# Kernel tuning notes

Measured on AMD Instinct MI355X. Metric: run time of the kernel, lower is better.

Reference implementation:

```python
import jax, jax.numpy as jnp
import numpy as np

N = 50000          # nodes
E = 1_600_000      # edges (avg degree 32)
FEAT = 128         # nfeat == nhid
HID = 128
L = 3              # nconvs
C = 10             # nclass
G = 128            # graphs in batch
BN_EPS = 1e-5


def setup_inputs() -> dict:
    key = jax.random.key(0)
    ks = jax.random.split(key, 8)
    x = jax.random.normal(ks[0], (N, FEAT), dtype=jnp.float32)
    edge_index = jax.random.randint(ks[1], (2, E), 0, N, dtype=jnp.int64)
    batch = jnp.sort(jax.random.randint(ks[2], (N,), 0, G, dtype=jnp.int64))
    # stacked per-layer MLP params (nfeat == nhid so shapes are uniform)
    W1 = jax.random.normal(ks[3], (L, FEAT, HID), dtype=jnp.float32) * 0.05
    b1 = jnp.zeros((L, HID), dtype=jnp.float32)
    W2 = jax.random.normal(ks[4], (L, HID, HID), dtype=jnp.float32) * 0.05
    b2 = jnp.zeros((L, HID), dtype=jnp.float32)
    # BatchNorm (eval mode: running stats)
    gamma = jnp.ones((L, HID), dtype=jnp.float32)
    beta = jnp.zeros((L, HID), dtype=jnp.float32)
    rmean = jnp.zeros((L, HID), dtype=jnp.float32)
    rvar = jnp.ones((L, HID), dtype=jnp.float32)
    fc_w = jax.random.normal(ks[5], (HID, C), dtype=jnp.float32) * 0.05
    fc_b = jnp.zeros((C,), dtype=jnp.float32)
    return {
        "x": x, "edge_index": edge_index, "batch": batch,
        "W1": W1, "b1": b1, "W2": W2, "b2": b2,
        "gamma": gamma, "beta": beta, "rmean": rmean, "rvar": rvar,
        "fc_w": fc_w, "fc_b": fc_b,
    }


def reference(x, edge_index, batch, W1, b1, W2, b2, gamma, beta, rmean, rvar, fc_w, fc_b):
    src, dst = edge_index[0], edge_index[1]
    for l in range(L):
        # GINConv aggregation: h_i = (1 + eps) * x_i + sum_{j -> i} x_j  (eps = 0)
        agg = jax.ops.segment_sum(x[src], dst, num_segments=N)  # [N, d] scatter-add
        h = x + agg
        # MLP: Linear -> ReLU -> Linear -> BatchNorm (eval: running stats)
        h = jax.nn.relu(h @ W1[l] + b1[l])
        h = h @ W2[l] + b2[l]
        h = (h - rmean[l]) * jax.lax.rsqrt(rvar[l] + BN_EPS) * gamma[l] + beta[l]
        # outer ReLU; dropout is identity at inference
        x = jax.nn.relu(h)
    # global mean pool over batch ids
    counts = jax.ops.segment_sum(jnp.ones((N,), x.dtype), batch, num_segments=G)
    pooled = jax.ops.segment_sum(x, batch, num_segments=G)
    pooled = pooled / jnp.clip(counts, 1.0)[:, None]  # [G, HID]
    logits = pooled @ fc_w + fc_b                      # [G, C]
    return jax.nn.log_softmax(logits, axis=1)
```

## Files before the change

kernel.cpp:

```cpp
#include <hip/hip_runtime.h>

#define NN 50000
#define EE 1600000
#define GG 128
#define NC 10

#define SB_N   49
#define SB_PAD 36864
#define BK_N   782
#define BK_PAD 2560
#define CHUNK  4096
#define NBLK1  391
#define SLICES 9

typedef __attribute__((ext_vector_type(8))) short bf16x8;
typedef __attribute__((ext_vector_type(4))) float f32x4;
typedef unsigned short u16;

__device__ inline u16 f2bf(float x){
  unsigned u = __builtin_bit_cast(unsigned, x);
  u += 0x7fffu + ((u >> 16) & 1u);
  return (u16)(u >> 16);
}
__device__ inline float bf2f(u16 u){
  return __builtin_bit_cast(float, ((unsigned)u) << 16);
}

__global__ void k_zero_int(int* __restrict__ p, int n){
  int i = blockIdx.x * 256 + threadIdx.x;
  if (i < n) p[i] = 0;
}

__global__ __launch_bounds__(256) void k_scatL1(const int* __restrict__ srcI, const int* __restrict__ dstI,
                                                int* __restrict__ scur, int* __restrict__ sstg){
  __shared__ int hist[SB_N];
  __shared__ int base[64];
  __shared__ int gadj[SB_N];
  __shared__ unsigned reo[CHUNK];
  int t = threadIdx.x;
  int e0 = blockIdx.x * CHUNK;
  int cnt = EE - e0; if (cnt > CHUNK) cnt = CHUNK;
  if (t < SB_N) hist[t] = 0;
  __syncthreads();
  unsigned p[16]; int rk[16];
  #pragma unroll
  for (int r = 0; r < 16; ++r){
    int i = r * 256 + t;
    if (i < cnt){
      unsigned d = (unsigned)dstI[e0 + i];
      p[r] = (d << 16) | (unsigned)srcI[e0 + i];
      rk[r] = atomicAdd(&hist[d >> 10], 1);
    }
  }
  __syncthreads();
  if (t < 64) base[t] = (t < SB_N) ? hist[t] : 0;
  __syncthreads();
  for (int off = 1; off < 64; off <<= 1){
    int a = (t < 64 && t >= off) ? base[t - off] : 0;
    __syncthreads();
    if (t < 64) base[t] += a;
    __syncthreads();
  }
  if (t < SB_N){
    int ex = base[t] - hist[t];
    gadj[t] = atomicAdd(&scur[t], hist[t]) - ex;
  }
  __syncthreads();
  #pragma unroll
  for (int r = 0; r < 16; ++r){
    int i = r * 256 + t;
    if (i < cnt){
      unsigned sb = p[r] >> 26;
      reo[(base[sb] - hist[sb]) + rk[r]] = p[r];
    }
  }
  __syncthreads();
  for (int q = t; q < cnt; q += 256){
    unsigned v = reo[q];
    unsigned sb = v >> 26;
    int off = gadj[sb] + q;
    if ((unsigned)off < SB_PAD) sstg[sb * SB_PAD + off] = (int)v;
  }
}

__global__ __launch_bounds__(256) void k_scatL2(const int* __restrict__ sstg, const int* __restrict__ scur,
                                                int* __restrict__ bcur, int* __restrict__ bstg){
  __shared__ int hist[16];
  __shared__ int base[16];
  __shared__ int gadj[16];
  __shared__ unsigned reo[CHUNK];
  int t = threadIdx.x;
  int sb = blockIdx.x / SLICES;
  int sl = blockIdx.x % SLICES;
  int ssz = scur[sb]; if (ssz > SB_PAD) ssz = SB_PAD;
  int i0 = sl * CHUNK;
  int cnt = ssz - i0;
  if (cnt <= 0) return;
  if (cnt > CHUNK) cnt = CHUNK;
  if (t < 16) hist[t] = 0;
  __syncthreads();
  unsigned p[16]; int rk[16];
  #pragma unroll
  for (int r = 0; r < 16; ++r){
    int i = r * 256 + t;
    if (i < cnt){
      p[r] = (unsigned)sstg[sb * SB_PAD + i0 + i];
      rk[r] = atomicAdd(&hist[(p[r] >> 22) & 15], 1);
    }
  }
  __syncthreads();
  if (t < 16) base[t] = hist[t];
  __syncthreads();
  for (int off = 1; off < 16; off <<= 1){
    int a = (t < 16 && t >= off) ? base[t - off] : 0;
    __syncthreads();
    if (t < 16) base[t] += a;
    __syncthreads();
  }
  if (t < 16){
    int ex = base[t] - hist[t];
    gadj[t] = atomicAdd(&bcur[sb * 16 + t], hist[t]) - ex;
  }
  __syncthreads();
  #pragma unroll
  for (int r = 0; r < 16; ++r){
    int i = r * 256 + t;
    if (i < cnt){
      unsigned b = (p[r] >> 22) & 15;
      reo[(base[b] - hist[b]) + rk[r]] = p[r];
    }
  }
  __syncthreads();
  for (int q = t; q < cnt; q += 256){
    unsigned v = reo[q];
    unsigned b = (v >> 22) & 15;
    int off = gadj[b] + q;
    if ((unsigned)off < BK_PAD) bstg[(sb * 16 + b) * BK_PAD + off] = (int)v;
  }
}

__global__ __launch_bounds__(256) void k_finalize(const int* __restrict__ bstg, const int* __restrict__ bcur,
                                                  u16* __restrict__ adj, int2* __restrict__ ndinfo){
  __shared__ unsigned ebuf[BK_PAD];
  __shared__ int hist[64];
  __shared__ int lrs[64];
  __shared__ int lcur[64];
  int b = blockIdx.x;
  int t = threadIdx.x;
  int bsz = bcur[b]; if (bsz > BK_PAD) bsz = BK_PAD;
  if (t < 64) hist[t] = 0;
  __syncthreads();
  for (int i = t; i < bsz; i += 256){
    unsigned p = (unsigned)bstg[b * BK_PAD + i];
    ebuf[i] = p;
    atomicAdd(&hist[(p >> 16) & 63], 1);
  }
  __syncthreads();
  if (t < 64) lrs[t] = hist[t];
  __syncthreads();
  for (int off = 1; off < 64; off <<= 1){
    int a = (t < 64 && t >= off) ? lrs[t - off] : 0;
    __syncthreads();
    if (t < 64) lrs[t] += a;
    __syncthreads();
  }
  if (t < 64){
    int ex = lrs[t] - hist[t];
    lcur[t] = ex;
    int node = b * 64 + t;
    if (node < NN) ndinfo[node] = make_int2(b * BK_PAD + ex, hist[t]);
  }
  __syncthreads();
  for (int i = t; i < bsz; i += 256){
    unsigned p = ebuf[i];
    int slot = atomicAdd(&lcur[(p >> 16) & 63], 1);
    adj[b * BK_PAD + slot] = (u16)(p & 0xffffu);
  }
}

__global__ void k_cvt_x(const float* __restrict__ x, u16* __restrict__ xb){
  int i = blockIdx.x * 256 + threadIdx.x;
  float4 v = ((const float4*)x)[i];
  ushort4 o;
  o.x = f2bf(v.x); o.y = f2bf(v.y); o.z = f2bf(v.z); o.w = f2bf(v.w);
  ((ushort4*)xb)[i] = o;
}

__global__ void k_prep_w(const float* __restrict__ W1, const float* __restrict__ W2,
                         u16* __restrict__ Wt){
  int i = blockIdx.x * 256 + threadIdx.x;
  int a = i >> 14; int r = i & 16383; int n = r >> 7; int k = r & 127;
  const float* Wsrc = (a < 3) ? (W1 + a * 16384) : (W2 + (a - 3) * 16384);
  Wt[a * 16384 + n * 128 + k] = f2bf(Wsrc[k * 128 + n]);
}

__global__ void k_prep_scsh(const float* __restrict__ b1, const float* __restrict__ b2,
                            const float* __restrict__ gma, const float* __restrict__ bta,
                            const float* __restrict__ rmn, const float* __restrict__ rvr,
                            float* __restrict__ SC, float* __restrict__ SH){
  int i = blockIdx.x * 256 + threadIdx.x;
  if (i < 768){
    int l = i >> 8; int r = i & 255; int mode = r >> 7; int c = r & 127;
    if (mode == 0){
      SC[(l * 2) * 128 + c] = 1.0f;
      SH[(l * 2) * 128 + c] = b1[l * 128 + c];
    } else {
      float S = gma[l * 128 + c] * rsqrtf(rvr[l * 128 + c] + 1e-5f);
      SC[(l * 2 + 1) * 128 + c] = S;
      SH[(l * 2 + 1) * 128 + c] = (b2[l * 128 + c] - rmn[l * 128 + c]) * S + bta[l * 128 + c];
    }
  }
}

__global__ __launch_bounds__(256) void k_agg(const u16* __restrict__ xb, u16* __restrict__ hb,
                                             const u16* __restrict__ adj,
                                             const int2* __restrict__ ndinfo){
  int t = threadIdx.x;
  int node = blockIdx.x * 16 + (t >> 4);
  int lane = t & 15;
  const bf16x8* xv = (const bf16x8*)xb;
  bf16x8 sv = xv[(long)node * 16 + lane];
  float a[8];
  #pragma unroll
  for (int j = 0; j < 8; ++j) a[j] = bf2f((u16)sv[j]);
  int2 nd = ndinfo[node];
  int r0 = nd.x;
  int d  = nd.y;
  int j = 0;
  for (; j + 4 <= d; j += 4){
    int s0 = adj[r0 + j + 0];
    int s1 = adj[r0 + j + 1];
    int s2 = adj[r0 + j + 2];
    int s3 = adj[r0 + j + 3];
    bf16x8 v0 = xv[(long)s0 * 16 + lane];
    bf16x8 v1 = xv[(long)s1 * 16 + lane];
    bf16x8 v2 = xv[(long)s2 * 16 + lane];
    bf16x8 v3 = xv[(long)s3 * 16 + lane];
    #pragma unroll
    for (int q = 0; q < 8; ++q)
      a[q] += bf2f((u16)v0[q]) + bf2f((u16)v1[q]) + bf2f((u16)v2[q]) + bf2f((u16)v3[q]);
  }
  for (; j < d; ++j){
    int s0 = adj[r0 + j];
    bf16x8 v0 = xv[(long)s0 * 16 + lane];
    #pragma unroll
    for (int q = 0; q < 8; ++q) a[q] += bf2f((u16)v0[q]);
  }
  bf16x8 o;
  #pragma unroll
  for (int j2 = 0; j2 < 8; ++j2) o[j2] = (short)f2bf(a[j2]);
  ((bf16x8*)hb)[(long)node * 16 + lane] = o;
}

__global__ __launch_bounds__(256, 2) void k_gemm(const u16* __restrict__ Ain,
                                                 const u16* __restrict__ Wt,
                                                 const float* __restrict__ SC,
                                                 const float* __restrict__ SH,
                                                 u16* __restrict__ Out){
  int gw = (blockIdx.x * 256 + threadIdx.x) >> 6;
  int l  = threadIdx.x & 63;
  int m  = l & 15;
  int kb = l >> 4;
  const int NW = (gridDim.x * 256) >> 6;

  bf16x8 w[8][4];
  #pragma unroll
  for (int mt = 0; mt < 8; ++mt)
    #pragma unroll
    for (int ks = 0; ks < 4; ++ks)
      w[mt][ks] = *(const bf16x8*)(Wt + (mt * 16 + m) * 128 + ks * 32 + kb * 8);

  for (int tile = gw; tile < 3125; tile += NW){
    long row0 = (long)tile * 16;
    f32x4 acc[8] = {};
    #pragma unroll
    for (int ks = 0; ks < 4; ++ks){
      bf16x8 h = *(const bf16x8*)(Ain + (row0 + m) * 128 + ks * 32 + kb * 8);
      #pragma unroll
      for (int mt = 0; mt < 8; ++mt)
        acc[mt] = __builtin_amdgcn_mfma_f32_16x16x32_bf16(w[mt][ks], h, acc[mt], 0, 0, 0);
    }
    #pragma unroll
    for (int mt = 0; mt < 8; ++mt){
      int c0 = mt * 16 + kb * 4;
      float4 sc = *(const float4*)(SC + c0);
      float4 sh = *(const float4*)(SH + c0);
      float v0 = fmaxf(acc[mt][0] * sc.x + sh.x, 0.f);
      float v1 = fmaxf(acc[mt][1] * sc.y + sh.y, 0.f);
      float v2 = fmaxf(acc[mt][2] * sc.z + sh.z, 0.f);
      float v3 = fmaxf(acc[mt][3] * sc.w + sh.w, 0.f);
      ushort4 o;
      o.x = f2bf(v0); o.y = f2bf(v1); o.z = f2bf(v2); o.w = f2bf(v3);
      *(ushort4*)(Out + (row0 + m) * 128 + c0) = o;
    }
  }
}

__global__ __launch_bounds__(256) void k_pool(const u16* __restrict__ xb,
                                              const int* __restrict__ batch,
                                              float* __restrict__ pooled){
  __shared__ float4 red[8][32];
  int b = blockIdx.x;
  int n0 = b << 6;
  int t = threadIdx.x;
  int lane = t & 31;
  int rg = t >> 5;
  int g0 = batch[n0];
  int lastn = n0 + 63; if (lastn >= NN) lastn = NN - 1;
  int nk = batch[lastn] - g0;
  const ushort4* xv = (const ushort4*)xb;
  float4 a0 = {0,0,0,0}, a1 = {0,0,0,0}, a2 = {0,0,0,0};
  int rbase = n0 + rg * 8;
  #pragma unroll
  for (int i = 0; i < 8; ++i){
    int r = rbase + i;
    if (r >= NN) break;
    int k = batch[r] - g0;
    ushort4 v = xv[(long)r * 32 + lane];
    float fx = bf2f(v.x), fy = bf2f(v.y), fz = bf2f(v.z), fw = bf2f(v.w);
    if (k == 0){ a0.x += fx; a0.y += fy; a0.z += fz; a0.w += fw; }
    else if (k == 1){ a1.x += fx; a1.y += fy; a1.z += fz; a1.w += fw; }
    else if (k == 2){ a2.x += fx; a2.y += fy; a2.z += fz; a2.w += fw; }
    else {
      float* pg = pooled + (g0 + k) * 128 + lane * 4;
      atomicAdd(pg + 0, fx); atomicAdd(pg + 1, fy);
      atomicAdd(pg + 2, fz); atomicAdd(pg + 3, fw);
    }
  }
  int kmax = (nk < 2) ? nk : 2;
  for (int k = 0; k <= kmax; ++k){
    red[rg][lane] = (k == 0) ? a0 : ((k == 1) ? a1 : a2);
    __syncthreads();
    if (t < 32){
      float4 s = red[0][t];
      #pragma unroll
      for (int r = 1; r < 8; ++r){
        float4 q = red[r][t];
        s.x += q.x; s.y += q.y; s.z += q.z; s.w += q.w;
      }
      float* pg = pooled + (g0 + k) * 128 + t * 4;
      atomicAdd(pg + 0, s.x); atomicAdd(pg + 1, s.y);
      atomicAdd(pg + 2, s.z); atomicAdd(pg + 3, s.w);
    }
    __syncthreads();
  }
}

__global__ void k_head(const float* __restrict__ pooled, const float* __restrict__ fcw,
                       const float* __restrict__ fcb, const int* __restrict__ batch,
                       float* __restrict__ out){
  int g = threadIdx.x;
  int lo, hi;
  { int a = 0, b = NN; while (a < b){ int mm = (a + b) >> 1; if (batch[mm] < g) a = mm + 1; else b = mm; } lo = a; }
  { int a = lo, b = NN; while (a < b){ int mm = (a + b) >> 1; if (batch[mm] < g + 1) a = mm + 1; else b = mm; } hi = a; }
  float inv = 1.0f / fmaxf((float)(hi - lo), 1.0f);
  float logit[NC];
  #pragma unroll
  for (int c = 0; c < NC; ++c) logit[c] = fcb[c];
  for (int k = 0; k < 128; ++k){
    float pv = pooled[g * 128 + k] * inv;
    #pragma unroll
    for (int c = 0; c < NC; ++c) logit[c] += pv * fcw[k * NC + c];
  }
  float m = logit[0];
  #pragma unroll
  for (int c = 1; c < NC; ++c) m = fmaxf(m, logit[c]);
  float sum = 0.f;
  #pragma unroll
  for (int c = 0; c < NC; ++c) sum += expf(logit[c] - m);
  float ls = logf(sum);
  #pragma unroll
  for (int c = 0; c < NC; ++c) out[g * NC + c] = logit[c] - m - ls;
}

extern "C" void kernel_launch(void* const* d_in, const int* in_sizes, int n_in,
                              void* d_out, int out_size, void* d_ws, size_t ws_size,
                              hipStream_t stream) {
  const float* x     = (const float*)d_in[0];
  const int*   eidx  = (const int*)  d_in[1];
  const int*   batch = (const int*)  d_in[2];
  const float* W1    = (const float*)d_in[3];
  const float* b1    = (const float*)d_in[4];
  const float* W2    = (const float*)d_in[5];
  const float* b2    = (const float*)d_in[6];
  const float* gma   = (const float*)d_in[7];
  const float* bta   = (const float*)d_in[8];
  const float* rmn   = (const float*)d_in[9];
  const float* rvr   = (const float*)d_in[10];
  const float* fcw   = (const float*)d_in[11];
  const float* fcb   = (const float*)d_in[12];
  float* out = (float*)d_out;

  const int* srcI = eidx;
  const int* dstI = eidx + EE;

  u16* bufX = (u16*)d_ws;
  u16* bufA = bufX + 6400000;
  u16* bufB = bufA + 6400000;
  u16* Wt   = bufB + 6400000;
  float* SC = (float*)(Wt + 98304);
  float* SH = SC + 768;
  float* pooled = SH + 768;
  int* ctr  = (int*)(pooled + 16384);
  int* scur = ctr;
  int* bcur = ctr + 64;
  u16* adj  = (u16*)(ctr + 848);
  int2* ndinfo = (int2*)(adj + (BK_N * BK_PAD));
  int* sstg = (int*)bufA;
  int* bstg = (int*)bufB;

  k_zero_int<<<68, 256, 0, stream>>>((int*)pooled, 16384 + 848);

  k_scatL1  <<<NBLK1, 256, 0, stream>>>(srcI, dstI, scur, sstg);
  k_scatL2  <<<SB_N * SLICES, 256, 0, stream>>>(sstg, scur, bcur, bstg);
  k_finalize<<<BK_N, 256, 0, stream>>>(bstg, bcur, adj, ndinfo);

  k_cvt_x    <<<6250, 256, 0, stream>>>(x, bufX);
  k_prep_w   <<<384, 256, 0, stream>>>(W1, W2, Wt);
  k_prep_scsh<<<3, 256, 0, stream>>>(b1, b2, gma, bta, rmn, rvr, SC, SH);

  u16* aggin [3] = { bufX, bufA, bufB };
  u16* aggout[3] = { bufA, bufB, bufA };
  u16* g0out [3] = { bufB, bufX, bufX };
  u16* g1out [3] = { bufA, bufB, bufA };

  for (int l = 0; l < 3; ++l){
    k_agg <<<3125, 256, 0, stream>>>(aggin[l], aggout[l], adj, ndinfo);
    k_gemm<<<256, 256, 0, stream>>>(aggout[l], Wt + l * 16384,
                                    SC + (l * 2) * 128, SH + (l * 2) * 128, g0out[l]);
    k_gemm<<<256, 256, 0, stream>>>(g0out[l], Wt + (3 + l) * 16384,
                                    SC + (l * 2 + 1) * 128, SH + (l * 2 + 1) * 128, g1out[l]);
  }

  k_pool<<<BK_N, 256, 0, stream>>>(g1out[2], batch, pooled);
  k_head<<<1, 128, 0, stream>>>(pooled, fcw, fcb, batch, out);
}
```

Baseline: 416.5 us.

## Fuse both MLP GEMMs per layer with pooling and merge prep kernels

Result: slower. 473.0 us (+13.6%).

```diff
diff --git a/kernel.cpp b/kernel.cpp
--- a/kernel.cpp
+++ b/kernel.cpp
@@ -178,36 +178,36 @@
   }
 }
 
-__global__ void k_cvt_x(const float* __restrict__ x, u16* __restrict__ xb){
-  int i = blockIdx.x * 256 + threadIdx.x;
-  float4 v = ((const float4*)x)[i];
-  ushort4 o;
-  o.x = f2bf(v.x); o.y = f2bf(v.y); o.z = f2bf(v.z); o.w = f2bf(v.w);
-  ((ushort4*)xb)[i] = o;
-}
-
-__global__ void k_prep_w(const float* __restrict__ W1, const float* __restrict__ W2,
-                         u16* __restrict__ Wt){
-  int i = blockIdx.x * 256 + threadIdx.x;
-  int a = i >> 14; int r = i & 16383; int n = r >> 7; int k = r & 127;
-  const float* Wsrc = (a < 3) ? (W1 + a * 16384) : (W2 + (a - 3) * 16384);
-  Wt[a * 16384 + n * 128 + k] = f2bf(Wsrc[k * 128 + n]);
-}
-
-__global__ void k_prep_scsh(const float* __restrict__ b1, const float* __restrict__ b2,
-                            const float* __restrict__ gma, const float* __restrict__ bta,
-                            const float* __restrict__ rmn, const float* __restrict__ rvr,
-                            float* __restrict__ SC, float* __restrict__ SH){
-  int i = blockIdx.x * 256 + threadIdx.x;
-  if (i < 768){
-    int l = i >> 8; int r = i & 255; int mode = r >> 7; int c = r & 127;
-    if (mode == 0){
-      SC[(l * 2) * 128 + c] = 1.0f;
-      SH[(l * 2) * 128 + c] = b1[l * 128 + c];
-    } else {
-      float S = gma[l * 128 + c] * rsqrtf(rvr[l * 128 + c] + 1e-5f);
-      SC[(l * 2 + 1) * 128 + c] = S;
-      SH[(l * 2 + 1) * 128 + c] = (b2[l * 128 + c] - rmn[l * 128 + c]) * S + bta[l * 128 + c];
+__global__ void k_prep(const float* __restrict__ x, const float* __restrict__ W1f, const float* __restrict__ W2f,
+                       const float* __restrict__ b1, const float* __restrict__ b2,
+                       const float* __restrict__ gma, const float* __restrict__ bta,
+                       const float* __restrict__ rmn, const float* __restrict__ rvr,
+                       u16* __restrict__ xb, u16* __restrict__ Wt,
+                       float* __restrict__ SC, float* __restrict__ SH){
+  int bid = blockIdx.x;
+  int t = threadIdx.x;
+  if (bid < 6250){
+    int i = bid * 256 + t;
+    float4 v = ((const float4*)x)[i];
+    ushort4 o;
+    o.x = f2bf(v.x); o.y = f2bf(v.y); o.z = f2bf(v.z); o.w = f2bf(v.w);
+    ((ushort4*)xb)[i] = o;
+  } else if (bid < 6634){
+    int i = (bid - 6250) * 256 + t;
+    int a = i >> 14; int r = i & 16383; int n = r >> 7; int k = r & 127;
+    const float* Wsrc = (a < 3) ? (W1f + a * 16384) : (W2f + (a - 3) * 16384);
+    Wt[a * 16384 + n * 128 + k] = f2bf(Wsrc[k * 128 + n]);
+  } else {
+    for (int i = t; i < 768; i += 256){
+      int l = i >> 8; int r = i & 255; int mode = r >> 7; int c = r & 127;
+      if (mode == 0){
+        SC[(l * 2) * 128 + c] = 1.0f;
+        SH[(l * 2) * 128 + c] = b1[l * 128 + c];
+      } else {
+        float S = gma[l * 128 + c] * rsqrtf(rvr[l * 128 + c] + 1e-5f);
+        SC[(l * 2 + 1) * 128 + c] = S;
+        SH[(l * 2 + 1) * 128 + c] = (b2[l * 128 + c] - rmn[l * 128 + c]) * S + bta[l * 128 + c];
+      }
     }
   }
 }
@@ -227,22 +227,33 @@
   int r0 = nd.x;
   int d  = nd.y;
   int j = 0;
+  for (; j + 8 <= d; j += 8){
+    bf16x8 v[8];
+    #pragma unroll
+    for (int u = 0; u < 8; ++u){
+      int s = adj[r0 + j + u];
+      v[u] = xv[(long)s * 16 + lane];
+    }
+    #pragma unroll
+    for (int q = 0; q < 8; ++q){
+      float s01 = bf2f((u16)v[0][q]) + bf2f((u16)v[1][q]);
+      float s23 = bf2f((u16)v[2][q]) + bf2f((u16)v[3][q]);
+      float s45 = bf2f((u16)v[4][q]) + bf2f((u16)v[5][q]);
+      float s67 = bf2f((u16)v[6][q]) + bf2f((u16)v[7][q]);
+      a[q] += (s01 + s23) + (s45 + s67);
+    }
+  }
   for (; j + 4 <= d; j += 4){
-    int s0 = adj[r0 + j + 0];
-    int s1 = adj[r0 + j + 1];
-    int s2 = adj[r0 + j + 2];
-    int s3 = adj[r0 + j + 3];
-    bf16x8 v0 = xv[(long)s0 * 16 + lane];
-    bf16x8 v1 = xv[(long)s1 * 16 + lane];
-    bf16x8 v2 = xv[(long)s2 * 16 + lane];
-    bf16x8 v3 = xv[(long)s3 * 16 + lane];
+    bf16x8 v0 = xv[(long)adj[r0 + j + 0] * 16 + lane];
+    bf16x8 v1 = xv[(long)adj[r0 + j + 1] * 16 + lane];
+    bf16x8 v2 = xv[(long)adj[r0 + j + 2] * 16 + lane];
+    bf16x8 v3 = xv[(long)adj[r0 + j + 3] * 16 + lane];
     #pragma unroll
     for (int q = 0; q < 8; ++q)
-      a[q] += bf2f((u16)v0[q]) + bf2f((u16)v1[q]) + bf2f((u16)v2[q]) + bf2f((u16)v3[q]);
+      a[q] += (bf2f((u16)v0[q]) + bf2f((u16)v1[q])) + (bf2f((u16)v2[q]) + bf2f((u16)v3[q]));
   }
   for (; j < d; ++j){
-    int s0 = adj[r0 + j];
-    bf16x8 v0 = xv[(long)s0 * 16 + lane];
+    bf16x8 v0 = xv[(long)adj[r0 + j] * 16 + lane];
     #pragma unroll
     for (int q = 0; q < 8; ++q) a[q] += bf2f((u16)v0[q]);
   }
@@ -252,23 +263,48 @@
   ((bf16x8*)hb)[(long)node * 16 + lane] = o;
 }
 
-__global__ __launch_bounds__(256, 2) void k_gemm(const u16* __restrict__ Ain,
-                                                 const u16* __restrict__ Wt,
-                                                 const float* __restrict__ SC,
-                                                 const float* __restrict__ SH,
-                                                 u16* __restrict__ Out){
-  int gw = (blockIdx.x * 256 + threadIdx.x) >> 6;
-  int l  = threadIdx.x & 63;
+template<int POOL>
+__global__ __launch_bounds__(256, 2) void k_mlp(const u16* __restrict__ Ain,
+                                                const u16* __restrict__ Wt1,
+                                                const u16* __restrict__ Wt2,
+                                                const float* __restrict__ B1,
+                                                const float* __restrict__ SC2,
+                                                const float* __restrict__ SH2,
+                                                const int* __restrict__ batch,
+                                                u16* __restrict__ Out,
+                                                float* __restrict__ pooled){
+  __shared__ u16 W2s[16384];
+  __shared__ u16 Hs[4][16][128];
+  __shared__ float P1[128], P2[128], P3[128];
+  int t = threadIdx.x;
+
+  #pragma unroll
+  for (int i = 0; i < 8; ++i){
+    int c = t + 256 * i;
+    int r = c >> 4, cc = c & 15;
+    unsigned byte = (unsigned)(r * 256 + cc * 16) ^ (unsigned)((r & 7) << 4);
+    *(bf16x8*)((char*)W2s + byte) = *(const bf16x8*)(Wt2 + c * 8);
+  }
+  if (t < 128){ P1[t] = B1[t]; P2[t] = SC2[t]; P3[t] = SH2[t]; }
+
+  int wv = t >> 6;
+  int l  = t & 63;
   int m  = l & 15;
   int kb = l >> 4;
-  const int NW = (gridDim.x * 256) >> 6;
-
-  bf16x8 w[8][4];
+
+  bf16x8 w1[8][4];
   #pragma unroll
   for (int mt = 0; mt < 8; ++mt)
     #pragma unroll
     for (int ks = 0; ks < 4; ++ks)
-      w[mt][ks] = *(const bf16x8*)(Wt + (mt * 16 + m) * 128 + ks * 32 + kb * 8);
+      w1[mt][ks] = *(const bf16x8*)(Wt1 + (mt * 16 + m) * 128 + ks * 32 + kb * 8);
+
+  __syncthreads();
+
+  char* hs = (char*)&Hs[wv][0][0];
+  unsigned mswz = (unsigned)((m & 7) << 4);
+  int gw = blockIdx.x * 4 + wv;
+  const int NW = gridDim.x * 4;
 
   for (int tile = gw; tile < 3125; tile += NW){
     long row0 = (long)tile * 16;
@@ -278,71 +314,86 @@
       bf16x8 h = *(const bf16x8*)(Ain + (row0 + m) * 128 + ks * 32 + kb * 8);
       #pragma unroll
       for (int mt = 0; mt < 8; ++mt)
-        acc[mt] = __builtin_amdgcn_mfma_f32_16x16x32_bf16(w[mt][ks], h, acc[mt], 0, 0, 0);
+        acc[mt] = __builtin_amdgcn_mfma_f32_16x16x32_bf16(w1[mt][ks], h, acc[mt], 0, 0, 0);
     }
     #pragma unroll
     for (int mt = 0; mt < 8; ++mt){
       int c0 = mt * 16 + kb * 4;
-      float4 sc = *(const float4*)(SC + c0);
-      float4 sh = *(const float4*)(SH + c0);
-      float v0 = fmaxf(acc[mt][0] * sc.x + sh.x, 0.f);
-      float v1 = fmaxf(acc[mt][1] * sc.y + sh.y, 0.f);
-      float v2 = fmaxf(acc[mt][2] * sc.z + sh.z, 0.f);
-      float v3 = fmaxf(acc[mt][3] * sc.w + sh.w, 0.f);
+      float4 bb = *(const float4*)&P1[c0];
       ushort4 o;
-      o.x = f2bf(v0); o.y = f2bf(v1); o.z = f2bf(v2); o.w = f2bf(v3);
-      *(ushort4*)(Out + (row0 + m) * 128 + c0) = o;
-    }
-  }
-}
-
-__global__ __launch_bounds__(256) void k_pool(const u16* __restrict__ xb,
-                                              const int* __restrict__ batch,
-                                              float* __restrict__ pooled){
-  __shared__ float4 red[8][32];
-  int b = blockIdx.x;
-  int n0 = b << 6;
-  int t = threadIdx.x;
-  int lane = t & 31;
-  int rg = t >> 5;
-  int g0 = batch[n0];
-  int lastn = n0 + 63; if (lastn >= NN) lastn = NN - 1;
-  int nk = batch[lastn] - g0;
-  const ushort4* xv = (const ushort4*)xb;
-  float4 a0 = {0,0,0,0}, a1 = {0,0,0,0}, a2 = {0,0,0,0};
-  int rbase = n0 + rg * 8;
-  #pragma unroll
-  for (int i = 0; i < 8; ++i){
-    int r = rbase + i;
-    if (r >= NN) break;
-    int k = batch[r] - g0;
-    ushort4 v = xv[(long)r * 32 + lane];
-    float fx = bf2f(v.x), fy = bf2f(v.y), fz = bf2f(v.z), fw = bf2f(v.w);
-    if (k == 0){ a0.x += fx; a0.y += fy; a0.z += fz; a0.w += fw; }
-    else if (k == 1){ a1.x += fx; a1.y += fy; a1.z += fz; a1.w += fw; }
-    else if (k == 2){ a2.x += fx; a2.y += fy; a2.z += fz; a2.w += fw; }
-    else {
-      float* pg = pooled + (g0 + k) * 128 + lane * 4;
-      atomicAdd(pg + 0, fx); atomicAdd(pg + 1, fy);
-      atomicAdd(pg + 2, fz); atomicAdd(pg + 3, fw);
-    }
-  }
-  int kmax = (nk < 2) ? nk : 2;
-  for (int k = 0; k <= kmax; ++k){
-    red[rg][lane] = (k == 0) ? a0 : ((k == 1) ? a1 : a2);
-    __syncthreads();
-    if (t < 32){
-      float4 s = red[0][t];
+      o.x = f2bf(fmaxf(acc[mt][0] + bb.x, 0.f));
+      o.y = f2bf(fmaxf(acc[mt][1] + bb.y, 0.f));
+      o.z = f2bf(fmaxf(acc[mt][2] + bb.z, 0.f));
+      o.w = f2bf(fmaxf(acc[mt][3] + bb.w, 0.f));
+      unsigned byte = (unsigned)(m * 256 + c0 * 2) ^ mswz;
+      *(ushort4*)(hs + byte) = o;
+    }
+    f32x4 acc2[8] = {};
+    #pragma unroll
+    for (int ks = 0; ks < 4; ++ks){
+      unsigned hb_ = (unsigned)(m * 256 + ks * 64 + kb * 16) ^ mswz;
+      bf16x8 h2 = *(const bf16x8*)(hs + hb_);
       #pragma unroll
-      for (int r = 1; r < 8; ++r){
-        float4 q = red[r][t];
-        s.x += q.x; s.y += q.y; s.z += q.z; s.w += q.w;
+      for (int mt = 0; mt < 8; ++mt){
+        unsigned wb = (unsigned)((mt * 16 + m) * 256 + ks * 64 + kb * 16) ^ mswz;
+        bf16x8 w2 = *(const bf16x8*)((char*)W2s + wb);
+        acc2[mt] = __builtin_amdgcn_mfma_f32_16x16x32_bf16(w2, h2, acc2[mt], 0, 0, 0);
       }
-      float* pg = pooled + (g0 + k) * 128 + t * 4;
-      atomicAdd(pg + 0, s.x); atomicAdd(pg + 1, s.y);
-      atomicAdd(pg + 2, s.z); atomicAdd(pg + 3, s.w);
-    }
-    __syncthreads();
+    }
+    if (!POOL){
+      #pragma unroll
+      for (int mt = 0; mt < 8; ++mt){
+        int c0 = mt * 16 + kb * 4;
+        float4 sc = *(const float4*)&P2[c0];
+        float4 sh = *(const float4*)&P3[c0];
+        ushort4 o;
+        o.x = f2bf(fmaxf(acc2[mt][0] * sc.x + sh.x, 0.f));
+        o.y = f2bf(fmaxf(acc2[mt][1] * sc.y + sh.y, 0.f));
+        o.z = f2bf(fmaxf(acc2[mt][2] * sc.z + sh.z, 0.f));
+        o.w = f2bf(fmaxf(acc2[mt][3] * sc.w + sh.w, 0.f));
+        *(ushort4*)(Out + (row0 + m) * 128 + c0) = o;
+      }
+    } else {
+      int b0 = batch[row0];
+      int b15 = batch[row0 + 15];
+      if (b0 == b15){
+        #pragma unroll
+        for (int mt = 0; mt < 8; ++mt){
+          int c0 = mt * 16 + kb * 4;
+          float4 sc = *(const float4*)&P2[c0];
+          float4 sh = *(const float4*)&P3[c0];
+          float v0 = fmaxf(acc2[mt][0] * sc.x + sh.x, 0.f);
+          float v1 = fmaxf(acc2[mt][1] * sc.y + sh.y, 0.f);
+          float v2 = fmaxf(acc2[mt][2] * sc.z + sh.z, 0.f);
+          float v3 = fmaxf(acc2[mt][3] * sc.w + sh.w, 0.f);
+          #pragma unroll
+          for (int off = 1; off < 16; off <<= 1){
+            v0 += __shfl_xor(v0, off);
+            v1 += __shfl_xor(v1, off);
+            v2 += __shfl_xor(v2, off);
+            v3 += __shfl_xor(v3, off);
+          }
+          if (m == 0){
+            float* pg = pooled + b0 * 128 + c0;
+            atomicAdd(pg + 0, v0); atomicAdd(pg + 1, v1);
+            atomicAdd(pg + 2, v2); atomicAdd(pg + 3, v3);
+          }
+        }
+      } else {
+        int bm = batch[row0 + m];
+        #pragma unroll
+        for (int mt = 0; mt < 8; ++mt){
+          int c0 = mt * 16 + kb * 4;
+          float4 sc = *(const float4*)&P2[c0];
+          float4 sh = *(const float4*)&P3[c0];
+          float* pg = pooled + bm * 128 + c0;
+          atomicAdd(pg + 0, fmaxf(acc2[mt][0] * sc.x + sh.x, 0.f));
+          atomicAdd(pg + 1, fmaxf(acc2[mt][1] * sc.y + sh.y, 0.f));
+          atomicAdd(pg + 2, fmaxf(acc2[mt][2] * sc.z + sh.z, 0.f));
+          atomicAdd(pg + 3, fmaxf(acc2[mt][3] * sc.w + sh.w, 0.f));
+        }
+      }
+    }
   }
 }
 
@@ -415,23 +466,17 @@
   k_scatL2  <<<SB_N * SLICES, 256, 0, stream>>>(sstg, scur, bcur, bstg);
   k_finalize<<<BK_N, 256, 0, stream>>>(bstg, bcur, adj, ndinfo);
 
-  k_cvt_x    <<<6250, 256, 0, stream>>>(x, bufX);
-  k_prep_w   <<<384, 256, 0, stream>>>(W1, W2, Wt);
-  k_prep_scsh<<<3, 256, 0, stream>>>(b1, b2, gma, bta, rmn, rvr, SC, SH);
-
-  u16* aggin [3] = { bufX, bufA, bufB };
-  u16* aggout[3] = { bufA, bufB, bufA };
-  u16* g0out [3] = { bufB, bufX, bufX };
-  u16* g1out [3] = { bufA, bufB, bufA };
-
-  for (int l = 0; l < 3; ++l){
-    k_agg <<<3125, 256, 0, stream>>>(aggin[l], aggout[l], adj, ndinfo);
-    k_gemm<<<256, 256, 0, stream>>>(aggout[l], Wt + l * 16384,
-                                    SC + (l * 2) * 128, SH + (l * 2) * 128, g0out[l]);
-    k_gemm<<<256, 256, 0, stream>>>(g0out[l], Wt + (3 + l) * 16384,
-                                    SC + (l * 2 + 1) * 128, SH + (l * 2 + 1) * 128, g1out[l]);
-  }
-
-  k_pool<<<BK_N, 256, 0, stream>>>(g1out[2], batch, pooled);
+  k_prep<<<6635, 256, 0, stream>>>(x, W1, W2, b1, b2, gma, bta, rmn, rvr, bufX, Wt, SC, SH);
+
+  k_agg   <<<3125, 256, 0, stream>>>(bufX, bufA, adj, ndinfo);
+  k_mlp<0><<<391, 256, 0, stream>>>(bufA, Wt + 0 * 16384, Wt + 3 * 16384,
+                                    SH + 0 * 128, SC + 1 * 128, SH + 1 * 128, batch, bufB, pooled);
+  k_agg   <<<3125, 256, 0, stream>>>(bufB, bufA, adj, ndinfo);
+  k_mlp<0><<<391, 256, 0, stream>>>(bufA, Wt + 1 * 16384, Wt + 4 * 16384,
+                                    SH + 2 * 128, SC + 3 * 128, SH + 3 * 128, batch, bufB, pooled);
+  k_agg   <<<3125, 256, 0, stream>>>(bufB, bufA, adj, ndinfo);
+  k_mlp<1><<<391, 256, 0, stream>>>(bufA, Wt + 2 * 16384, Wt + 5 * 16384,
+                                    SH + 4 * 128, SC + 5 * 128, SH + 5 * 128, batch, bufB, pooled);
+
   k_head<<<1, 128, 0, stream>>>(pooled, fcw, fcb, batch, out);
 }
```
